# Kernel optimization log

Hardware: AMD Instinct MI355X
Metric: run time of the kernel (lower is better)

## Reference

```python
import jax, jax.numpy as jnp
import numpy as np


def setup_inputs() -> dict:
    key = jax.random.key(0)
    k1, k2, k3, k4 = jax.random.split(key, 4)
    B, T, C, H = 4, 2048, 1024, 64
    x = jax.random.normal(k1, (B, T, C), dtype=jnp.float32)
    # Linear(embed_dim, head_size, bias=False) weights, stored as [C, H] for x @ W
    s = 1.0 / np.sqrt(C)
    Wq = jax.random.normal(k2, (C, H), dtype=jnp.float32) * s
    Wk = jax.random.normal(k3, (C, H), dtype=jnp.float32) * s
    Wv = jax.random.normal(k4, (C, H), dtype=jnp.float32) * s
    return {"x": x, "Wq": Wq, "Wk": Wk, "Wv": Wv}


def reference(x, Wq, Wk, Wv):
    B, T, C = x.shape
    q = x @ Wq  # [B, T, H]
    k = x @ Wk
    v = x @ Wv
    # NOTE: original scales by embed_dim**-0.5 (C), not head_size**-0.5
    scale = C ** (-0.5)
    wei = jnp.einsum("bqh,bkh->bqk", q, k) * scale  # [B, T, T]
    causal = jnp.tril(jnp.ones((T, T), dtype=bool))
    wei = jnp.where(causal, wei, -jnp.inf)
    wei = jax.nn.softmax(wei, axis=-1)
    # dropout_rate = 0 -> identity
    out = jnp.einsum("bqk,bkh->bqh", wei, v)  # [B, T, H]
    return out
```

## Files before the change

### kernel.cpp

```cpp
#include <hip/hip_runtime.h>
#include <hip/hip_bf16.h>
#include <cmath>

#define B_ 4
#define T_ 2048
#define C_ 1024
#define H_ 64
#define K2_ 0.04508422003f
#define THRRAW_ 177.0f
#define NEG_ -3.0e38f

typedef __attribute__((ext_vector_type(4))) float f32x4;
typedef __attribute__((ext_vector_type(8))) short s16x8;
typedef __attribute__((ext_vector_type(4))) unsigned short u16x4;
typedef __attribute__((ext_vector_type(8))) unsigned short u16x8;

__device__ inline unsigned short f2bf(float f) {
    union { __hip_bfloat16 h; unsigned short u; } cv;
    cv.h = __float2bfloat16(f);
    return cv.u;
}

#define LDK 72

__global__ __launch_bounds__(256) void wprep(
    const float* __restrict__ Wq, const float* __restrict__ Wk,
    const float* __restrict__ Wv, unsigned short* __restrict__ wt)
{
    const int g = blockIdx.x * 256 + threadIdx.x;
    const int c = g >> 7;
    const int kg = (g & 127) * 8;
    const float* W = (c < 64) ? Wq : (c < 128) ? Wk : Wv;
    const int col = c & 63;
    u16x4 a, b;
    a.x = f2bf(W[(size_t)(kg + 0) * H_ + col]);
    a.y = f2bf(W[(size_t)(kg + 1) * H_ + col]);
    a.z = f2bf(W[(size_t)(kg + 2) * H_ + col]);
    a.w = f2bf(W[(size_t)(kg + 3) * H_ + col]);
    b.x = f2bf(W[(size_t)(kg + 4) * H_ + col]);
    b.y = f2bf(W[(size_t)(kg + 5) * H_ + col]);
    b.z = f2bf(W[(size_t)(kg + 6) * H_ + col]);
    b.w = f2bf(W[(size_t)(kg + 7) * H_ + col]);
    *(u16x4*)&wt[(size_t)c * C_ + kg] = a;
    *(u16x4*)&wt[(size_t)c * C_ + kg + 4] = b;
}

__global__ __launch_bounds__(256, 4) void proj_dbuf(
    const float* __restrict__ x, const unsigned short* __restrict__ wt,
    unsigned short* __restrict__ qb, unsigned short* __restrict__ kb,
    unsigned short* __restrict__ vt)
{
    __shared__ alignas(16) unsigned short As[2][64 * LDK];
    __shared__ alignas(16) unsigned short Bs[2][64 * LDK];

    const int t = threadIdx.x, lane = t & 63, w = t >> 6;
    const int blk = blockIdx.x;
    const int mat = blk % 3;
    const int row0 = (blk / 3) * 64;
    const int wr = (w >> 1) * 32, wc = (w & 1) * 32;
    const int fr = lane & 15, ko = (lane >> 4) * 8;

    const int ar0 = t >> 4, akc = (t & 15) * 4;
    const int bc0 = t >> 3, bkc = (t & 7) * 8;

    const float* xp = x + (size_t)(row0 + ar0) * C_ + akc;
    const unsigned short* wp = wt + (size_t)(mat * 64 + bc0) * C_ + bkc;

    f32x4 pa[4];
    u16x8 pb[2];

    #pragma unroll
    for (int i = 0; i < 4; ++i) pa[i] = *(const f32x4*)(xp + (size_t)i * 16 * C_);
    #pragma unroll
    for (int i = 0; i < 2; ++i) pb[i] = *(const u16x8*)(wp + (size_t)i * 32 * C_);
    #pragma unroll
    for (int i = 0; i < 4; ++i) {
        u16x4 bv;
        bv.x = f2bf(pa[i].x); bv.y = f2bf(pa[i].y);
        bv.z = f2bf(pa[i].z); bv.w = f2bf(pa[i].w);
        *(u16x4*)&As[0][(ar0 + i * 16) * LDK + akc] = bv;
    }
    #pragma unroll
    for (int i = 0; i < 2; ++i)
        *(u16x8*)&Bs[0][(bc0 + i * 32) * LDK + bkc] = pb[i];

    f32x4 acc[2][2];
    #pragma unroll
    for (int mi = 0; mi < 2; ++mi)
        #pragma unroll
        for (int ni = 0; ni < 2; ++ni)
            acc[mi][ni] = (f32x4){0.f, 0.f, 0.f, 0.f};

    for (int it = 0; it < 16; ++it) {
        __syncthreads();
        const int cur = it & 1;
        if (it < 15) {
            const float* xn = xp + (it + 1) * 64;
            const unsigned short* wn = wp + (it + 1) * 64;
            #pragma unroll
            for (int i = 0; i < 4; ++i) pa[i] = *(const f32x4*)(xn + (size_t)i * 16 * C_);
            #pragma unroll
            for (int i = 0; i < 2; ++i) pb[i] = *(const u16x8*)(wn + (size_t)i * 32 * C_);
        }
        const unsigned short* A = &As[cur][0];
        const unsigned short* Bb = &Bs[cur][0];
        #pragma unroll
        for (int ks = 0; ks < 2; ++ks) {
            s16x8 a0 = *(const s16x8*)&A[(wr + fr) * LDK + ks * 32 + ko];
            s16x8 a1 = *(const s16x8*)&A[(wr + 16 + fr) * LDK + ks * 32 + ko];
            s16x8 b0 = *(const s16x8*)&Bb[(wc + fr) * LDK + ks * 32 + ko];
            s16x8 b1 = *(const s16x8*)&Bb[(wc + 16 + fr) * LDK + ks * 32 + ko];
            acc[0][0] = __builtin_amdgcn_mfma_f32_16x16x32_bf16(a0, b0, acc[0][0], 0, 0, 0);
            acc[0][1] = __builtin_amdgcn_mfma_f32_16x16x32_bf16(a0, b1, acc[0][1], 0, 0, 0);
            acc[1][0] = __builtin_amdgcn_mfma_f32_16x16x32_bf16(a1, b0, acc[1][0], 0, 0, 0);
            acc[1][1] = __builtin_amdgcn_mfma_f32_16x16x32_bf16(a1, b1, acc[1][1], 0, 0, 0);
        }
        if (it < 15) {
            const int nxt = cur ^ 1;
            #pragma unroll
            for (int i = 0; i < 4; ++i) {
                u16x4 bv;
                bv.x = f2bf(pa[i].x); bv.y = f2bf(pa[i].y);
                bv.z = f2bf(pa[i].z); bv.w = f2bf(pa[i].w);
                *(u16x4*)&As[nxt][(ar0 + i * 16) * LDK + akc] = bv;
            }
            #pragma unroll
            for (int i = 0; i < 2; ++i)
                *(u16x8*)&Bs[nxt][(bc0 + i * 32) * LDK + bkc] = pb[i];
        }
    }

    if (mat < 2) {
        unsigned short* outb = (mat == 0) ? qb : kb;
        #pragma unroll
        for (int mi = 0; mi < 2; ++mi)
            #pragma unroll
            for (int ni = 0; ni < 2; ++ni)
                #pragma unroll
                for (int j = 0; j < 4; ++j) {
                    int row = row0 + wr + mi * 16 + (lane >> 4) * 4 + j;
                    int col = wc + ni * 16 + fr;
                    outb[(size_t)row * H_ + col] = f2bf(acc[mi][ni][j]);
                }
    } else {
        __syncthreads();
        unsigned short* Tr = &As[0][0];
        #pragma unroll
        for (int mi = 0; mi < 2; ++mi)
            #pragma unroll
            for (int ni = 0; ni < 2; ++ni)
                #pragma unroll
                for (int j = 0; j < 4; ++j) {
                    int r = wr + mi * 16 + (lane >> 4) * 4 + j;
                    int cc = wc + ni * 16 + fr;
                    Tr[cc * LDK + r] = f2bf(acc[mi][ni][j]);
                }
        __syncthreads();
        int h = t >> 2, c0 = (t & 3) * 16;
        int bb = row0 >> 11, trow = row0 & 2047;
        s16x8 v0 = *(const s16x8*)&Tr[h * LDK + c0];
        s16x8 v1 = *(const s16x8*)&Tr[h * LDK + c0 + 8];
        size_t dst = (size_t)bb * H_ * T_ + (size_t)h * T_ + trow + c0;
        *(s16x8*)&vt[dst] = v0;
        *(s16x8*)&vt[dst + 8] = v1;
    }
}

__global__ __launch_bounds__(512, 4) void attn_mfma(
    const unsigned short* __restrict__ qb, const unsigned short* __restrict__ kb,
    const unsigned short* __restrict__ vt, float* __restrict__ out)
{
    __shared__ alignas(16) unsigned short Ps[8][1024];
    __shared__ float Os[8][16][68];
    __shared__ float Mm[8][16];
    __shared__ float Ll[8][16];

    const int t = threadIdx.x, lane = t & 63, w = t >> 6;
    const int fr = lane & 15, hi4 = lane >> 4;
    const int blk = blockIdx.x;
    const int b = blk & 3;
    const int qt = 127 - (blk >> 2);
    const int qbase = qt * 16;

    const unsigned short* qp = qb + ((size_t)b * T_ + qbase) * H_;
    const unsigned short* kp = kb + (size_t)b * T_ * H_;
    const unsigned short* vp = vt + (size_t)b * H_ * T_;

    s16x8 qf0 = *(const s16x8*)&qp[fr * H_ + hi4 * 8];
    s16x8 qf1 = *(const s16x8*)&qp[fr * H_ + 32 + hi4 * 8];

    const int nt = (qbase + 79) >> 6;
    const int per = (nt + 7) >> 3;
    const int tb = w * per;
    int te = tb + per; if (te > nt) te = nt;

    float m = NEG_, l = 0.f;
    f32x4 o[4];
    #pragma unroll
    for (int hf = 0; hf < 4; ++hf) o[hf] = (f32x4){0.f, 0.f, 0.f, 0.f};

    unsigned short* P = &Ps[w][0];
    const int swz = (fr & 3) << 4;
    const int qrow = qbase + fr;

    for (int kt = tb; kt < te; ++kt) {
        const int kt0 = kt << 6;

        f32x4 s[4];
        #pragma unroll
        for (int n = 0; n < 4; ++n) {
            const unsigned short* kr = &kp[(size_t)(kt0 + n * 16 + fr) * H_ + hi4 * 8];
            s16x8 kf0 = *(const s16x8*)kr;
            s16x8 kf1 = *(const s16x8*)(kr + 32);
            f32x4 a = (f32x4){0.f, 0.f, 0.f, 0.f};
            a = __builtin_amdgcn_mfma_f32_16x16x32_bf16(kf0, qf0, a, 0, 0, 0);
            a = __builtin_amdgcn_mfma_f32_16x16x32_bf16(kf1, qf1, a, 0, 0, 0);
            s[n] = a;
        }

        s16x8 vf[4][2];
        #pragma unroll
        for (int hf = 0; hf < 4; ++hf) {
            const unsigned short* vr = &vp[(size_t)(hf * 16 + fr) * T_ + kt0 + hi4 * 8];
            vf[hf][0] = *(const s16x8*)vr;
            vf[hf][1] = *(const s16x8*)(vr + 32);
        }

        if (kt0 + 63 > qbase) {
            #pragma unroll
            for (int n = 0; n < 4; ++n)
                #pragma unroll
                for (int j = 0; j < 4; ++j) {
                    int key = kt0 + n * 16 + hi4 * 4 + j;
                    s[n][j] = (key > qrow) ? NEG_ : s[n][j];
                }
        }

        float mxl = fmaxf(fmaxf(fmaxf(fmaxf(s[0][0], s[0][1]), fmaxf(s[0][2], s[0][3])),
                                fmaxf(fmaxf(s[1][0], s[1][1]), fmaxf(s[1][2], s[1][3]))),
                          fmaxf(fmaxf(fmaxf(s[2][0], s[2][1]), fmaxf(s[2][2], s[2][3])),
                                fmaxf(fmaxf(s[3][0], s[3][1]), fmaxf(s[3][2], s[3][3]))));
        if (!__all(mxl - m <= THRRAW_)) {
            float mx = fmaxf(mxl, __shfl_xor(mxl, 16));
            mx = fmaxf(mx, __shfl_xor(mx, 32));
            float mn = fmaxf(m, mx);
            float corr = exp2f((m - mn) * K2_);
            m = mn;
            l *= corr;
            #pragma unroll
            for (int j = 0; j < 4; ++j) {
                float cj = __shfl(corr, (lane & 48) + hi4 * 4 + j);
                o[0][j] *= cj; o[1][j] *= cj; o[2][j] *= cj; o[3][j] *= cj;
            }
        }
        const float nmk = -m * K2_;
        float sum = 0.f;
        #pragma unroll
        for (int n = 0; n < 4; ++n)
            #pragma unroll
            for (int j = 0; j < 4; ++j) {
                float p = exp2f(fmaf(s[n][j], K2_, nmk));
                s[n][j] = p; sum += p;
            }
        sum += __shfl_xor(sum, 16);
        sum += __shfl_xor(sum, 32);
        l += sum;

        #pragma unroll
        for (int n = 0; n < 4; ++n) {
            u16x4 pk;
            pk.x = f2bf(s[n][0]); pk.y = f2bf(s[n][1]);
            pk.z = f2bf(s[n][2]); pk.w = f2bf(s[n][3]);
            *(u16x4*)&P[fr * 64 + ((n * 16 + hi4 * 4) ^ swz)] = pk;
        }
        s16x8 pa0 = *(const s16x8*)&P[fr * 64 + ((hi4 * 8) ^ swz)];
        s16x8 pa1 = *(const s16x8*)&P[fr * 64 + ((32 + hi4 * 8) ^ swz)];

        #pragma unroll
        for (int hf = 0; hf < 4; ++hf) {
            o[hf] = __builtin_amdgcn_mfma_f32_16x16x32_bf16(pa0, vf[hf][0], o[hf], 0, 0, 0);
            o[hf] = __builtin_amdgcn_mfma_f32_16x16x32_bf16(pa1, vf[hf][1], o[hf], 0, 0, 0);
        }
    }

    if (hi4 == 0) { Mm[w][fr] = m; Ll[w][fr] = l; }
    #pragma unroll
    for (int hf = 0; hf < 4; ++hf)
        #pragma unroll
        for (int j = 0; j < 4; ++j)
            Os[w][hi4 * 4 + j][hf * 16 + fr] = o[hf][j];
    __syncthreads();

    if (t < 256) {
        int qq = t >> 4, h0 = (t & 15) * 4;
        float M = NEG_;
        #pragma unroll
        for (int s8 = 0; s8 < 8; ++s8) M = fmaxf(M, Mm[s8][qq]);
        float L = 0.f;
        f32x4 r = (f32x4){0.f, 0.f, 0.f, 0.f};
        #pragma unroll
        for (int s8 = 0; s8 < 8; ++s8) {
            float e = exp2f((Mm[s8][qq] - M) * K2_);
            L += Ll[s8][qq] * e;
            f32x4 osv = *(const f32x4*)&Os[s8][qq][h0];
            r.x = fmaf(osv.x, e, r.x);
            r.y = fmaf(osv.y, e, r.y);
            r.z = fmaf(osv.z, e, r.z);
            r.w = fmaf(osv.w, e, r.w);
        }
        float il = 1.0f / L;
        r.x *= il; r.y *= il; r.z *= il; r.w *= il;
        *(f32x4*)&out[((size_t)b * T_ + qbase + qq) * H_ + h0] = r;
    }
}

extern "C" void kernel_launch(void* const* d_in, const int* in_sizes, int n_in,
                              void* d_out, int out_size, void* d_ws, size_t ws_size,
                              hipStream_t stream) {
    const float* x  = (const float*)d_in[0];
    const float* Wq = (const float*)d_in[1];
    const float* Wk = (const float*)d_in[2];
    const float* Wv = (const float*)d_in[3];
    float* outp = (float*)d_out;

    unsigned short* base = (unsigned short*)d_ws;
    unsigned short* qbw = base;
    unsigned short* kbw = base + 524288;
    unsigned short* vtw = base + 1048576;
    unsigned short* wtw = base + 1572864;

    wprep<<<96, 256, 0, stream>>>(Wq, Wk, Wv, wtw);
    proj_dbuf<<<(B_ * T_ / 64) * 3, 256, 0, stream>>>(x, wtw, qbw, kbw, vtw);
    attn_mfma<<<B_ * (T_ / 16), 512, 0, stream>>>(qbw, kbw, vtw, outp);
}
```

Baseline: 50.20 us.

## Halve projection row tile and restructure attention shared memory and pointers

The projection kernel now uses 32-row tiles, launching twice as many blocks with half the MFMA work per wave, and writes the V transpose through a 40-stride scratch. The attention kernel overlays the P and O scratch buffers in one shared union with a barrier between uses, pads the P rows to 72, and walks K and V with incrementing pointers instead of recomputing addresses each tile. The aim is more parallelism in the projection stage, less LDS per block, and fewer bank conflicts and address calculations. In exchange each projection block reuses less data and the attention epilogue gains an extra __syncthreads.

```diff
diff --git a/kernel.cpp b/kernel.cpp
--- a/kernel.cpp
+++ b/kernel.cpp
@@ -45,19 +45,19 @@
     *(u16x4*)&wt[(size_t)c * C_ + kg + 4] = b;
 }
 
-__global__ __launch_bounds__(256, 4) void proj_dbuf(
+__global__ __launch_bounds__(256, 4) void proj32(
     const float* __restrict__ x, const unsigned short* __restrict__ wt,
     unsigned short* __restrict__ qb, unsigned short* __restrict__ kb,
     unsigned short* __restrict__ vt)
 {
-    __shared__ alignas(16) unsigned short As[2][64 * LDK];
+    __shared__ alignas(16) unsigned short As[2][32 * LDK];
     __shared__ alignas(16) unsigned short Bs[2][64 * LDK];
 
     const int t = threadIdx.x, lane = t & 63, w = t >> 6;
     const int blk = blockIdx.x;
     const int mat = blk % 3;
-    const int row0 = (blk / 3) * 64;
-    const int wr = (w >> 1) * 32, wc = (w & 1) * 32;
+    const int row0 = (blk / 3) * 32;
+    const int wr = (w >> 1) * 16, wc = (w & 1) * 32;
     const int fr = lane & 15, ko = (lane >> 4) * 8;
 
     const int ar0 = t >> 4, akc = (t & 15) * 4;
@@ -66,30 +66,25 @@
     const float* xp = x + (size_t)(row0 + ar0) * C_ + akc;
     const unsigned short* wp = wt + (size_t)(mat * 64 + bc0) * C_ + bkc;
 
-    f32x4 pa[4];
+    f32x4 pa[2];
     u16x8 pb[2];
 
+    pa[0] = *(const f32x4*)(xp);
+    pa[1] = *(const f32x4*)(xp + (size_t)16 * C_);
+    pb[0] = *(const u16x8*)(wp);
+    pb[1] = *(const u16x8*)(wp + (size_t)32 * C_);
     #pragma unroll
-    for (int i = 0; i < 4; ++i) pa[i] = *(const f32x4*)(xp + (size_t)i * 16 * C_);
-    #pragma unroll
-    for (int i = 0; i < 2; ++i) pb[i] = *(const u16x8*)(wp + (size_t)i * 32 * C_);
-    #pragma unroll
-    for (int i = 0; i < 4; ++i) {
+    for (int i = 0; i < 2; ++i) {
         u16x4 bv;
         bv.x = f2bf(pa[i].x); bv.y = f2bf(pa[i].y);
         bv.z = f2bf(pa[i].z); bv.w = f2bf(pa[i].w);
         *(u16x4*)&As[0][(ar0 + i * 16) * LDK + akc] = bv;
-    }
-    #pragma unroll
-    for (int i = 0; i < 2; ++i)
         *(u16x8*)&Bs[0][(bc0 + i * 32) * LDK + bkc] = pb[i];
-
-    f32x4 acc[2][2];
-    #pragma unroll
-    for (int mi = 0; mi < 2; ++mi)
-        #pragma unroll
-        for (int ni = 0; ni < 2; ++ni)
-            acc[mi][ni] = (f32x4){0.f, 0.f, 0.f, 0.f};
+    }
+
+    f32x4 acc[2];
+    acc[0] = (f32x4){0.f, 0.f, 0.f, 0.f};
+    acc[1] = (f32x4){0.f, 0.f, 0.f, 0.f};
 
     for (int it = 0; it < 16; ++it) {
         __syncthreads();
@@ -97,72 +92,61 @@
         if (it < 15) {
             const float* xn = xp + (it + 1) * 64;
             const unsigned short* wn = wp + (it + 1) * 64;
-            #pragma unroll
-            for (int i = 0; i < 4; ++i) pa[i] = *(const f32x4*)(xn + (size_t)i * 16 * C_);
-            #pragma unroll
-            for (int i = 0; i < 2; ++i) pb[i] = *(const u16x8*)(wn + (size_t)i * 32 * C_);
+            pa[0] = *(const f32x4*)(xn);
+            pa[1] = *(const f32x4*)(xn + (size_t)16 * C_);
+            pb[0] = *(const u16x8*)(wn);
+            pb[1] = *(const u16x8*)(wn + (size_t)32 * C_);
         }
         const unsigned short* A = &As[cur][0];
         const unsigned short* Bb = &Bs[cur][0];
         #pragma unroll
         for (int ks = 0; ks < 2; ++ks) {
             s16x8 a0 = *(const s16x8*)&A[(wr + fr) * LDK + ks * 32 + ko];
-            s16x8 a1 = *(const s16x8*)&A[(wr + 16 + fr) * LDK + ks * 32 + ko];
             s16x8 b0 = *(const s16x8*)&Bb[(wc + fr) * LDK + ks * 32 + ko];
             s16x8 b1 = *(const s16x8*)&Bb[(wc + 16 + fr) * LDK + ks * 32 + ko];
-            acc[0][0] = __builtin_amdgcn_mfma_f32_16x16x32_bf16(a0, b0, acc[0][0], 0, 0, 0);
-            acc[0][1] = __builtin_amdgcn_mfma_f32_16x16x32_bf16(a0, b1, acc[0][1], 0, 0, 0);
-            acc[1][0] = __builtin_amdgcn_mfma_f32_16x16x32_bf16(a1, b0, acc[1][0], 0, 0, 0);
-            acc[1][1] = __builtin_amdgcn_mfma_f32_16x16x32_bf16(a1, b1, acc[1][1], 0, 0, 0);
+            acc[0] = __builtin_amdgcn_mfma_f32_16x16x32_bf16(a0, b0, acc[0], 0, 0, 0);
+            acc[1] = __builtin_amdgcn_mfma_f32_16x16x32_bf16(a0, b1, acc[1], 0, 0, 0);
         }
         if (it < 15) {
             const int nxt = cur ^ 1;
             #pragma unroll
-            for (int i = 0; i < 4; ++i) {
+            for (int i = 0; i < 2; ++i) {
                 u16x4 bv;
                 bv.x = f2bf(pa[i].x); bv.y = f2bf(pa[i].y);
                 bv.z = f2bf(pa[i].z); bv.w = f2bf(pa[i].w);
                 *(u16x4*)&As[nxt][(ar0 + i * 16) * LDK + akc] = bv;
-            }
-            #pragma unroll
-            for (int i = 0; i < 2; ++i)
                 *(u16x8*)&Bs[nxt][(bc0 + i * 32) * LDK + bkc] = pb[i];
-        }
-    }
-
+            }
+        }
+    }
+
+    const int hi4 = lane >> 4;
     if (mat < 2) {
         unsigned short* outb = (mat == 0) ? qb : kb;
         #pragma unroll
-        for (int mi = 0; mi < 2; ++mi)
-            #pragma unroll
-            for (int ni = 0; ni < 2; ++ni)
-                #pragma unroll
-                for (int j = 0; j < 4; ++j) {
-                    int row = row0 + wr + mi * 16 + (lane >> 4) * 4 + j;
-                    int col = wc + ni * 16 + fr;
-                    outb[(size_t)row * H_ + col] = f2bf(acc[mi][ni][j]);
-                }
+        for (int ni = 0; ni < 2; ++ni)
+            #pragma unroll
+            for (int j = 0; j < 4; ++j) {
+                int row = row0 + wr + hi4 * 4 + j;
+                int col = wc + ni * 16 + fr;
+                outb[(size_t)row * H_ + col] = f2bf(acc[ni][j]);
+            }
     } else {
         __syncthreads();
         unsigned short* Tr = &As[0][0];
         #pragma unroll
-        for (int mi = 0; mi < 2; ++mi)
-            #pragma unroll
-            for (int ni = 0; ni < 2; ++ni)
-                #pragma unroll
-                for (int j = 0; j < 4; ++j) {
-                    int r = wr + mi * 16 + (lane >> 4) * 4 + j;
-                    int cc = wc + ni * 16 + fr;
-                    Tr[cc * LDK + r] = f2bf(acc[mi][ni][j]);
-                }
+        for (int ni = 0; ni < 2; ++ni)
+            #pragma unroll
+            for (int j = 0; j < 4; ++j) {
+                int h = wc + ni * 16 + fr;
+                int r = wr + hi4 * 4 + j;
+                Tr[h * 40 + r] = f2bf(acc[ni][j]);
+            }
         __syncthreads();
-        int h = t >> 2, c0 = (t & 3) * 16;
+        int h = t >> 2, tg = (t & 3) * 8;
         int bb = row0 >> 11, trow = row0 & 2047;
-        s16x8 v0 = *(const s16x8*)&Tr[h * LDK + c0];
-        s16x8 v1 = *(const s16x8*)&Tr[h * LDK + c0 + 8];
-        size_t dst = (size_t)bb * H_ * T_ + (size_t)h * T_ + trow + c0;
-        *(s16x8*)&vt[dst] = v0;
-        *(s16x8*)&vt[dst + 8] = v1;
+        u16x8 vv = *(const u16x8*)&Tr[h * 40 + tg];
+        *(u16x8*)&vt[(size_t)bb * H_ * T_ + (size_t)h * T_ + trow + tg] = vv;
     }
 }
 
@@ -170,8 +154,7 @@
     const unsigned short* __restrict__ qb, const unsigned short* __restrict__ kb,
     const unsigned short* __restrict__ vt, float* __restrict__ out)
 {
-    __shared__ alignas(16) unsigned short Ps[8][1024];
-    __shared__ float Os[8][16][68];
+    __shared__ alignas(16) unsigned char UB[36864];
     __shared__ float Mm[8][16];
     __shared__ float Ll[8][16];
 
@@ -199,17 +182,24 @@
     #pragma unroll
     for (int hf = 0; hf < 4; ++hf) o[hf] = (f32x4){0.f, 0.f, 0.f, 0.f};
 
-    unsigned short* P = &Ps[w][0];
+    unsigned short* P = (unsigned short*)UB + w * 1152;
     const int swz = (fr & 3) << 4;
     const int qrow = qbase + fr;
 
+    const unsigned short* kp0 = kp + (size_t)tb * 4096 + fr * H_ + hi4 * 8;
+    const unsigned short* kp2 = kp0 + 2048;
+    const unsigned short* vq0 = vp + (size_t)(fr) * T_      + tb * 64 + hi4 * 8;
+    const unsigned short* vq1 = vp + (size_t)(16 + fr) * T_ + tb * 64 + hi4 * 8;
+    const unsigned short* vq2 = vp + (size_t)(32 + fr) * T_ + tb * 64 + hi4 * 8;
+    const unsigned short* vq3 = vp + (size_t)(48 + fr) * T_ + tb * 64 + hi4 * 8;
+
     for (int kt = tb; kt < te; ++kt) {
         const int kt0 = kt << 6;
 
         f32x4 s[4];
         #pragma unroll
         for (int n = 0; n < 4; ++n) {
-            const unsigned short* kr = &kp[(size_t)(kt0 + n * 16 + fr) * H_ + hi4 * 8];
+            const unsigned short* kr = ((n < 2) ? kp0 : kp2) + (n & 1) * 1024;
             s16x8 kf0 = *(const s16x8*)kr;
             s16x8 kf1 = *(const s16x8*)(kr + 32);
             f32x4 a = (f32x4){0.f, 0.f, 0.f, 0.f};
@@ -218,13 +208,13 @@
             s[n] = a;
         }
 
-        s16x8 vf[4][2];
-        #pragma unroll
-        for (int hf = 0; hf < 4; ++hf) {
-            const unsigned short* vr = &vp[(size_t)(hf * 16 + fr) * T_ + kt0 + hi4 * 8];
-            vf[hf][0] = *(const s16x8*)vr;
-            vf[hf][1] = *(const s16x8*)(vr + 32);
-        }
+        s16x8 vf0a = *(const s16x8*)vq0, vf0b = *(const s16x8*)(vq0 + 32);
+        s16x8 vf1a = *(const s16x8*)vq1, vf1b = *(const s16x8*)(vq1 + 32);
+        s16x8 vf2a = *(const s16x8*)vq2, vf2b = *(const s16x8*)(vq2 + 32);
+        s16x8 vf3a = *(const s16x8*)vq3, vf3b = *(const s16x8*)(vq3 + 32);
+
+        kp0 += 4096; kp2 += 4096;
+        vq0 += 64; vq1 += 64; vq2 += 64; vq3 += 64;
 
         if (kt0 + 63 > qbase) {
             #pragma unroll
@@ -271,24 +261,29 @@
             u16x4 pk;
             pk.x = f2bf(s[n][0]); pk.y = f2bf(s[n][1]);
             pk.z = f2bf(s[n][2]); pk.w = f2bf(s[n][3]);
-            *(u16x4*)&P[fr * 64 + ((n * 16 + hi4 * 4) ^ swz)] = pk;
-        }
-        s16x8 pa0 = *(const s16x8*)&P[fr * 64 + ((hi4 * 8) ^ swz)];
-        s16x8 pa1 = *(const s16x8*)&P[fr * 64 + ((32 + hi4 * 8) ^ swz)];
-
-        #pragma unroll
-        for (int hf = 0; hf < 4; ++hf) {
-            o[hf] = __builtin_amdgcn_mfma_f32_16x16x32_bf16(pa0, vf[hf][0], o[hf], 0, 0, 0);
-            o[hf] = __builtin_amdgcn_mfma_f32_16x16x32_bf16(pa1, vf[hf][1], o[hf], 0, 0, 0);
-        }
-    }
-
+            *(u16x4*)&P[fr * 72 + ((n * 16 + hi4 * 4) ^ swz)] = pk;
+        }
+        s16x8 pa0 = *(const s16x8*)&P[fr * 72 + ((hi4 * 8) ^ swz)];
+        s16x8 pa1 = *(const s16x8*)&P[fr * 72 + ((32 + hi4 * 8) ^ swz)];
+
+        o[0] = __builtin_amdgcn_mfma_f32_16x16x32_bf16(pa0, vf0a, o[0], 0, 0, 0);
+        o[0] = __builtin_amdgcn_mfma_f32_16x16x32_bf16(pa1, vf0b, o[0], 0, 0, 0);
+        o[1] = __builtin_amdgcn_mfma_f32_16x16x32_bf16(pa0, vf1a, o[1], 0, 0, 0);
+        o[1] = __builtin_amdgcn_mfma_f32_16x16x32_bf16(pa1, vf1b, o[1], 0, 0, 0);
+        o[2] = __builtin_amdgcn_mfma_f32_16x16x32_bf16(pa0, vf2a, o[2], 0, 0, 0);
+        o[2] = __builtin_amdgcn_mfma_f32_16x16x32_bf16(pa1, vf2b, o[2], 0, 0, 0);
+        o[3] = __builtin_amdgcn_mfma_f32_16x16x32_bf16(pa0, vf3a, o[3], 0, 0, 0);
+        o[3] = __builtin_amdgcn_mfma_f32_16x16x32_bf16(pa1, vf3b, o[3], 0, 0, 0);
+    }
+
+    __syncthreads();
+    float* Ob = (float*)UB;
     if (hi4 == 0) { Mm[w][fr] = m; Ll[w][fr] = l; }
     #pragma unroll
     for (int hf = 0; hf < 4; ++hf)
         #pragma unroll
         for (int j = 0; j < 4; ++j)
-            Os[w][hi4 * 4 + j][hf * 16 + fr] = o[hf][j];
+            Ob[((size_t)w * 16 + hi4 * 4 + j) * 68 + hf * 16 + fr] = o[hf][j];
     __syncthreads();
 
     if (t < 256) {
@@ -302,7 +297,7 @@
         for (int s8 = 0; s8 < 8; ++s8) {
             float e = exp2f((Mm[s8][qq] - M) * K2_);
             L += Ll[s8][qq] * e;
-            f32x4 osv = *(const f32x4*)&Os[s8][qq][h0];
+            f32x4 osv = *(const f32x4*)&Ob[((size_t)s8 * 16 + qq) * 68 + h0];
             r.x = fmaf(osv.x, e, r.x);
             r.y = fmaf(osv.y, e, r.y);
             r.z = fmaf(osv.z, e, r.z);
@@ -330,6 +325,6 @@
     unsigned short* wtw = base + 1572864;
 
     wprep<<<96, 256, 0, stream>>>(Wq, Wk, Wv, wtw);
-    proj_dbuf<<<(B_ * T_ / 64) * 3, 256, 0, stream>>>(x, wtw, qbw, kbw, vtw);
+    proj32<<<(B_ * T_ / 32) * 3, 256, 0, stream>>>(x, wtw, qbw, kbw, vtw);
     attn_mfma<<<B_ * (T_ / 16), 512, 0, stream>>>(qbw, kbw, vtw, outp);
 }
```

After: 53.97 us. +7.5%, slower.
